# Performance work log

Measured on AMD Instinct MI355X. Metric: run time of the kernel, lower is better.

Reference implementation:

```python
import jax, jax.numpy as jnp
import numpy as np

B, S, D = 16, 4096, 64
N_HASHES, BUCKET_SIZE = 8, 64
TOKEN_SELF_ATTN_VALUE = -50000.0


def setup_inputs() -> dict:
    key = jax.random.key(0)
    k1, k2, k3 = jax.random.split(key, 3)
    qk = jax.random.normal(k1, (B, S, D), jnp.float32)
    v = jax.random.normal(k2, (B, S, D), jnp.float32)
    # random rotations for LSH hashing: (batch, dim, n_hashes, n_buckets//2)
    rotations = jax.random.normal(k3, (B, D, N_HASHES, (S // BUCKET_SIZE) // 2), jnp.float32)
    return {"qk": qk, "v": v, "rotations": rotations}


def _look_one_back(x):
    # concat each chunk with the previous chunk (wrapping): (b, c, n, ...) -> (b, c, 2n, ...)
    return jnp.concatenate([x, jnp.roll(x, 1, axis=1)], axis=2)


def _lsh_attention(qk, v, rotations):
    b, s, d = qk.shape
    n_buckets = s // BUCKET_SIZE
    # --- hash vectors (rehash_each_round=True path) ---
    rotated = jnp.einsum('btf,bfhi->bhti', qk, rotations)          # (b, h, s, nb/2)
    rotated = jnp.concatenate([rotated, -rotated], axis=-1)        # (b, h, s, nb)
    buckets = jnp.argmax(rotated, axis=-1)                          # (b, h, s)
    offsets = (jnp.arange(N_HASHES) * n_buckets)[None, :, None]
    buckets = (buckets + offsets).reshape(b, -1)                    # (b, h*s)
    # --- stable bucket sort of tokens ---
    ticker = jnp.arange(N_HASHES * s)[None, :]
    buckets_and_t = s * buckets + ticker % s
    sticker = jnp.argsort(buckets_and_t, axis=-1)                   # sorted order
    undo_sort = jnp.argsort(sticker, axis=-1)
    st = sticker % s                                                # original token index
    sqk = jnp.take_along_axis(qk, st[..., None], axis=1)            # (b, h*s, d)
    sv = jnp.take_along_axis(v, st[..., None], axis=1)
    chunk_size = N_HASHES * n_buckets
    bq_t = st.reshape(b, chunk_size, -1)                            # (b, c, n)
    bqk = sqk.reshape(b, chunk_size, -1, d)                         # (b, c, n, d)
    bv = sv.reshape(b, chunk_size, -1, d)
    # shared-QK: keys are L2-normalized queries
    norm = jnp.linalg.norm(bqk, axis=-1, keepdims=True)
    bk = bqk / jnp.maximum(norm, 1e-12)
    bk = _look_one_back(bk)                                         # (b, c, 2n, d)
    bvl = _look_one_back(bv)
    bkv_t = _look_one_back(bq_t)                                    # (b, c, 2n)
    dots = jnp.einsum('bhie,bhje->bhij', bqk, bk) * (d ** -0.5)     # (b, c, n, 2n)
    # mask self-attention (token attends to itself only as last resort)
    self_mask = bq_t[:, :, :, None] == bkv_t[:, :, None, :]
    dots = jnp.where(self_mask, TOKEN_SELF_ATTN_VALUE, dots)
    # stable softmax per chunk; keep logsumexp for cross-round combination
    lse = jax.nn.logsumexp(dots, axis=-1, keepdims=True)            # (b, c, n, 1)
    p = jnp.exp(dots - lse)
    bo = jnp.einsum('buij,buje->buie', p, bvl)                      # (b, c, n, d)
    so = bo.reshape(b, -1, d)                                       # (b, h*s, d)
    slogits = lse.reshape(b, -1)                                    # (b, h*s)
    # undo the sort
    o = jnp.take_along_axis(so, undo_sort[..., None], axis=1)
    logits = jnp.take_along_axis(slogits, undo_sort, axis=1)
    o = o.reshape(b, N_HASHES, s, d)
    logits = logits.reshape(b, N_HASHES, s, 1)
    # combine hash rounds weighted by softmax over per-round logsumexp
    probs = jnp.exp(logits - jax.nn.logsumexp(logits, axis=1, keepdims=True))
    return jnp.sum(o * probs, axis=1)                               # (b, s, d)


def reference(qk, v, rotations):
    return _lsh_attention(qk, v, rotations)
```

## Files before the change

### kernel.cpp

```cpp
#include <hip/hip_runtime.h>
#include <math.h>

#define NB_B 16
#define NB_S 4096
#define NB_D 64
#define NB_H 8

#define KSTR 72
#define PSTR 136
#define VSTR 72

typedef _Float16 half_t;
typedef __attribute__((ext_vector_type(2))) _Float16 half2t;
typedef __attribute__((ext_vector_type(4))) _Float16 half4;
typedef __attribute__((ext_vector_type(8))) _Float16 half8;
typedef __attribute__((ext_vector_type(4))) float floatx4;

__global__ __launch_bounds__(256) void prep_kernel(const float* __restrict__ qk,
                                                   const float* __restrict__ v,
                                                   half_t* __restrict__ khat,
                                                   half_t* __restrict__ vh,
                                                   float* __restrict__ norm) {
  int g = blockIdx.x * 256 + threadIdx.x;
  float4 qv = ((const float4*)qk)[g];
  float4 vv = ((const float4*)v)[g];
  float ss = qv.x * qv.x + qv.y * qv.y + qv.z * qv.z + qv.w * qv.w;
  for (int off = 1; off < 16; off <<= 1) ss += __shfl_xor(ss, off);
  float nr = fmaxf(sqrtf(ss), 1e-12f);
  float sc = 1.0f / nr;
  half4 hk = {(half_t)(qv.x * sc), (half_t)(qv.y * sc), (half_t)(qv.z * sc),
              (half_t)(qv.w * sc)};
  half4 hv = {(half_t)vv.x, (half_t)vv.y, (half_t)vv.z, (half_t)vv.w};
  ((half4*)khat)[g] = hk;
  ((half4*)vh)[g] = hv;
  if ((threadIdx.x & 15) == 0) norm[g >> 4] = nr;
}

__global__ __launch_bounds__(256) void hash_kernel(const float* __restrict__ qk,
                                                   const float* __restrict__ rot,
                                                   int* __restrict__ bkt) {
  __shared__ float rotS[64 * 32];
  int tid = threadIdx.x;
  int blk = blockIdx.x;
  int tile = blk & 15, bh = blk >> 4;
  int h = bh & 7, b = bh >> 3;
  int t = (tile << 8) + tid;

  for (int i = tid; i < 2048; i += 256) {
    int f = i >> 5, ii = i & 31;
    rotS[i] = rot[(((size_t)b * 64 + f) * 8 + h) * 32 + ii];
  }
  __syncthreads();

  const float4* qrow = (const float4*)(qk + (((size_t)b << 12) + t) * 64);
  float qreg[64];
#pragma unroll
  for (int j = 0; j < 16; j++) *(float4*)(qreg + 4 * j) = qrow[j];

  float acc[32];
#pragma unroll
  for (int i = 0; i < 32; i++) acc[i] = 0.f;

#pragma unroll
  for (int f = 0; f < 64; f++) {
    float qf = qreg[f];
#pragma unroll
    for (int i4 = 0; i4 < 8; i4++) {
      float4 w = *(const float4*)(rotS + f * 32 + i4 * 4);
      acc[i4 * 4 + 0] = __fadd_rn(acc[i4 * 4 + 0], __fmul_rn(qf, w.x));
      acc[i4 * 4 + 1] = __fadd_rn(acc[i4 * 4 + 1], __fmul_rn(qf, w.y));
      acc[i4 * 4 + 2] = __fadd_rn(acc[i4 * 4 + 2], __fmul_rn(qf, w.z));
      acc[i4 * 4 + 3] = __fadd_rn(acc[i4 * 4 + 3], __fmul_rn(qf, w.w));
    }
  }

  float b1 = acc[0];
  int i1 = 0;
#pragma unroll
  for (int i = 1; i < 32; i++)
    if (acc[i] > b1) { b1 = acc[i]; i1 = i; }
#pragma unroll
  for (int i = 0; i < 32; i++) {
    float x = -acc[i];
    if (x > b1) { b1 = x; i1 = 32 + i; }
  }
  bkt[(((size_t)(b * 8 + h)) << 12) + t] = i1;
}

__global__ __launch_bounds__(256) void sort_kernel(const int* __restrict__ bkt,
                                                   int* __restrict__ st) {
  __shared__ int lb[4096];
  __shared__ int hist[4096];
  __shared__ int cumoff[64];
  int tid = threadIdx.x;
  int b = blockIdx.x >> 3, h = blockIdx.x & 7;
  const int* gb = bkt + (((size_t)(b * 8 + h)) << 12);
  for (int t = tid; t < 4096; t += 256) lb[t] = gb[t];
  for (int i = tid; i < 4096; i += 256) hist[i] = 0;
  __syncthreads();
  for (int t = tid; t < 4096; t += 256) atomicAdd(&hist[((t >> 6) << 6) | lb[t]], 1);
  __syncthreads();
  if (tid < 64) {
    int run = 0;
    for (int cc = 0; cc < 64; cc++) {
      int x = hist[(cc << 6) | tid];
      hist[(cc << 6) | tid] = run;
      run += x;
    }
    int s = run;
    for (int off = 1; off < 64; off <<= 1) {
      int u = __shfl_up(s, off);
      if (tid >= off) s += u;
    }
    cumoff[tid] = s - run;
  }
  __syncthreads();
  int lane = tid & 63;
  for (int p = 0; p < 16; p++) {
    int t = (p << 8) + tid;
    int vb = lb[t];
    unsigned long long m = 0xFFFFFFFFFFFFFFFFull;
#pragma unroll
    for (int bit = 0; bit < 6; bit++) {
      unsigned long long bl = __ballot((vb >> bit) & 1);
      m &= ((vb >> bit) & 1) ? bl : ~bl;
    }
    int rank = __popcll(m & ((1ull << lane) - 1ull));
    int cpos = cumoff[vb] + hist[((t >> 6) << 6) | vb] + rank;
    st[(((size_t)(b * 8 + h)) << 12) + cpos] = t;
  }
}

__global__ __launch_bounds__(256) void chunk_kernel(const half_t* __restrict__ khat,
                                                    const half_t* __restrict__ vh,
                                                    const float* __restrict__ norm,
                                                    const int* __restrict__ st,
                                                    half_t* __restrict__ oh,
                                                    float* __restrict__ lse) {
  __shared__ __align__(16) half_t Ks[128 * KSTR];
  __shared__ __align__(16) half_t Vt[64 * VSTR];
  __shared__ int tk[128];
  __shared__ float normS[64];
  int tid = threadIdx.x;
  int g = blockIdx.x & 511;
  int b = blockIdx.x >> 9;
  int h = g >> 6, c = g & 63;
  int gp = (g + 511) & 511;
  int hp = gp >> 6, cp = gp & 63;
  if (tid < 64) {
    tk[tid] = st[(((size_t)(b * 8 + h)) << 12) + (c << 6) + tid];
  } else if (tid < 128) {
    tk[tid] = st[(((size_t)(b * 8 + hp)) << 12) + (cp << 6) + (tid - 64)];
  }
  __syncthreads();
  if (tid < 64) normS[tid] = norm[(b << 12) + tk[tid]];
  for (int idx = tid; idx < 1024; idx += 256) {
    int row = idx >> 3, fo = idx & 7;
    half8 val = *(const half8*)(khat + (((size_t)(b << 12) + tk[row]) << 6) + fo * 8);
    *(half8*)(Ks + row * KSTR + fo * 8) = val;
  }
  {
    int kp = tid & 31, ch = tid >> 5;
    half8 r0 = *(const half8*)(vh + (((size_t)(b << 12) + tk[2 * kp]) << 6) + ch * 8);
    half8 r1 = *(const half8*)(vh + (((size_t)(b << 12) + tk[2 * kp + 1]) << 6) + ch * 8);
#pragma unroll
    for (int j = 0; j < 8; j++) {
      half2t pr = {r0[j], r1[j]};
      *(half2t*)(Vt + (ch * 8 + j) * VSTR + 2 * kp) = pr;
    }
  }
  __syncthreads();

  int lane = tid & 63, w = tid >> 6;
  int m = lane & 15, quad = lane >> 4;
  half8 afr[2];
#pragma unroll
  for (int ki = 0; ki < 2; ki++)
    afr[ki] = *(const half8*)(Ks + (w * 16 + m) * KSTR + ki * 32 + quad * 8);
  int ti[4];
  float scr[4];
#pragma unroll
  for (int r = 0; r < 4; r++) {
    int rr = w * 16 + quad * 4 + r;
    ti[r] = tk[rr];
    scr[r] = 0.125f * normS[rr];
  }

  float d[8][4];
#pragma unroll
  for (int nt = 0; nt < 8; nt++) {
    floatx4 acc = {0.f, 0.f, 0.f, 0.f};
#pragma unroll
    for (int ki = 0; ki < 2; ki++) {
      half8 bfr = *(const half8*)(Ks + (nt * 16 + m) * KSTR + ki * 32 + quad * 8);
      acc = __builtin_amdgcn_mfma_f32_16x16x32_f16(afr[ki], bfr, acc, 0, 0, 0);
    }
    int tj = tk[nt * 16 + m];
#pragma unroll
    for (int r = 0; r < 4; r++)
      d[nt][r] = (ti[r] == tj) ? -50000.0f : acc[r] * scr[r];
  }

  float mr[4], lr[4];
#pragma unroll
  for (int r = 0; r < 4; r++) {
    float mm = d[0][r];
#pragma unroll
    for (int nt = 1; nt < 8; nt++) mm = fmaxf(mm, d[nt][r]);
    for (int off = 1; off < 16; off <<= 1) mm = fmaxf(mm, __shfl_xor(mm, off));
    float ll = 0.f;
#pragma unroll
    for (int nt = 0; nt < 8; nt++) ll += __expf(d[nt][r] - mm);
    for (int off = 1; off < 16; off <<= 1) ll += __shfl_xor(ll, off);
    mr[r] = mm;
    lr[r] = ll;
    if (m == 0) lse[(((size_t)(b * 8 + h)) << 12) + ti[r]] = mm + __logf(ll);
  }
  __syncthreads();

  half_t* Ps = Ks;
#pragma unroll
  for (int nt = 0; nt < 8; nt++) {
#pragma unroll
    for (int r = 0; r < 4; r++) {
      Ps[(w * 16 + quad * 4 + r) * PSTR + nt * 16 + m] = (half_t)__expf(d[nt][r] - mr[r]);
    }
  }
  __syncthreads();

  half8 pfr[4];
#pragma unroll
  for (int kk = 0; kk < 4; kk++)
    pfr[kk] = *(const half8*)(Ps + (w * 16 + m) * PSTR + kk * 32 + quad * 8);

  floatx4 accO[4];
#pragma unroll
  for (int dt = 0; dt < 4; dt++) accO[dt] = (floatx4){0.f, 0.f, 0.f, 0.f};

#pragma unroll
  for (int dt = 0; dt < 4; dt++) {
#pragma unroll
    for (int kk = 0; kk < 2; kk++) {
      half8 bfr = *(const half8*)(Vt + (dt * 16 + m) * VSTR + kk * 32 + quad * 8);
      accO[dt] = __builtin_amdgcn_mfma_f32_16x16x32_f16(pfr[kk], bfr, accO[dt], 0, 0, 0);
    }
  }
  __syncthreads();

  {
    int kp = tid & 31, ch = tid >> 5;
    half8 r0 = *(const half8*)(vh + (((size_t)(b << 12) + tk[64 + 2 * kp]) << 6) + ch * 8);
    half8 r1 = *(const half8*)(vh + (((size_t)(b << 12) + tk[65 + 2 * kp]) << 6) + ch * 8);
#pragma unroll
    for (int j = 0; j < 8; j++) {
      half2t pr = {r0[j], r1[j]};
      *(half2t*)(Vt + (ch * 8 + j) * VSTR + 2 * kp) = pr;
    }
  }
  __syncthreads();

#pragma unroll
  for (int dt = 0; dt < 4; dt++) {
#pragma unroll
    for (int kk = 2; kk < 4; kk++) {
      half8 bfr = *(const half8*)(Vt + (dt * 16 + m) * VSTR + (kk - 2) * 32 + quad * 8);
      accO[dt] = __builtin_amdgcn_mfma_f32_16x16x32_f16(pfr[kk], bfr, accO[dt], 0, 0, 0);
    }
  }
  __syncthreads();

  half_t* Ot = Vt;
#pragma unroll
  for (int r = 0; r < 4; r++) {
    float inv = 1.0f / lr[r];
#pragma unroll
    for (int dt = 0; dt < 4; dt++) {
      Ot[(w * 16 + quad * 4 + r) * VSTR + dt * 16 + m] = (half_t)(accO[dt][r] * inv);
    }
  }
  __syncthreads();
  for (int idx = tid; idx < 512; idx += 256) {
    int row = idx >> 3, fo = idx & 7;
    half8 val = *(const half8*)(Ot + row * VSTR + fo * 8);
    *(half8*)(oh + ((((size_t)(b * 8 + h)) << 12) + tk[row]) * 64 + fo * 8) = val;
  }
}

__global__ __launch_bounds__(256) void combine_kernel(const half_t* __restrict__ oh,
                                                      const float* __restrict__ lse,
                                                      float* __restrict__ out) {
  int idx = blockIdx.x * 256 + threadIdx.x;
  int do8 = idx & 7;
  int ts = idx >> 3;
  int b = ts >> 12, t = ts & 4095;
  size_t base = ((size_t)b << 15) + t;
  float L[8];
  float m = -3.4e38f;
#pragma unroll
  for (int h = 0; h < 8; h++) {
    L[h] = lse[base + ((size_t)h << 12)];
    m = fmaxf(m, L[h]);
  }
  float s = 0.f;
#pragma unroll
  for (int h = 0; h < 8; h++) s += __expf(L[h] - m);
  float lt = m + __logf(s);
  float acc[8];
#pragma unroll
  for (int j = 0; j < 8; j++) acc[j] = 0.f;
#pragma unroll
  for (int h = 0; h < 8; h++) {
    float wgt = __expf(L[h] - lt);
    half8 o = *(const half8*)(oh + ((base + ((size_t)h << 12)) << 6) + do8 * 8);
#pragma unroll
    for (int j = 0; j < 8; j++) acc[j] += wgt * (float)o[j];
  }
  float* dst = out + ((((size_t)b << 12) + t) << 6) + do8 * 8;
  *(float4*)dst = (float4){acc[0], acc[1], acc[2], acc[3]};
  *(float4*)(dst + 4) = (float4){acc[4], acc[5], acc[6], acc[7]};
}

extern "C" void kernel_launch(void* const* d_in, const int* in_sizes, int n_in,
                              void* d_out, int out_size, void* d_ws, size_t ws_size,
                              hipStream_t stream) {
  const float* qk = (const float*)d_in[0];
  const float* v = (const float*)d_in[1];
  const float* rot = (const float*)d_in[2];
  float* out = (float*)d_out;

  int* bkt = (int*)d_ws;
  int* stp = bkt + NB_B * NB_H * NB_S;
  float* lse = (float*)(stp + NB_B * NB_H * NB_S);
  float* norm = lse + NB_B * NB_H * NB_S;
  half_t* khat = (half_t*)(norm + NB_B * NB_S);
  half_t* vh = khat + (size_t)NB_B * NB_S * NB_D;
  half_t* oh = vh + (size_t)NB_B * NB_S * NB_D;

  prep_kernel<<<NB_B * NB_S * 16 / 256, 256, 0, stream>>>(qk, v, khat, vh, norm);
  hash_kernel<<<NB_B * NB_H * 16, 256, 0, stream>>>(qk, rot, bkt);
  sort_kernel<<<NB_B * NB_H, 256, 0, stream>>>(bkt, stp);
  chunk_kernel<<<NB_B * 512, 256, 0, stream>>>(khat, vh, norm, stp, oh, lse);
  combine_kernel<<<NB_B * NB_S * 8 / 256, 256, 0, stream>>>(oh, lse, out);
}
```

Baseline: 214.3 us.

## Preload both V halves, dedupe softmax exps, and hash two rounds per block

The chunk kernel now loads both halves of the look-back V tile into separate LDS buffers up front. This removes a mid-kernel global load and two barriers, and the redundant barrier after the per-wave P store is dropped. Softmax exponentials are computed once and reused for the row sum and the P matrix instead of being evaluated twice. The hash kernel handles two hash rounds per block, reusing the query registers and reading rotations straight from global memory with uniform addresses instead of staging them in LDS. In exchange it uses about 9 KB more LDS per chunk block and launches half as many hash blocks.

```diff
diff --git a/kernel.cpp b/kernel.cpp
--- a/kernel.cpp
+++ b/kernel.cpp
@@ -39,52 +39,52 @@
 __global__ __launch_bounds__(256) void hash_kernel(const float* __restrict__ qk,
                                                    const float* __restrict__ rot,
                                                    int* __restrict__ bkt) {
-  __shared__ float rotS[64 * 32];
   int tid = threadIdx.x;
   int blk = blockIdx.x;
-  int tile = blk & 15, bh = blk >> 4;
-  int h = bh & 7, b = bh >> 3;
+  int tile = blk & 15;
+  int bhp = blk >> 4;
+  int hp = bhp & 3, b = bhp >> 2;
   int t = (tile << 8) + tid;
-
-  for (int i = tid; i < 2048; i += 256) {
-    int f = i >> 5, ii = i & 31;
-    rotS[i] = rot[(((size_t)b * 64 + f) * 8 + h) * 32 + ii];
-  }
-  __syncthreads();
 
   const float4* qrow = (const float4*)(qk + (((size_t)b << 12) + t) * 64);
   float qreg[64];
 #pragma unroll
   for (int j = 0; j < 16; j++) *(float4*)(qreg + 4 * j) = qrow[j];
 
-  float acc[32];
-#pragma unroll
-  for (int i = 0; i < 32; i++) acc[i] = 0.f;
-
-#pragma unroll
-  for (int f = 0; f < 64; f++) {
-    float qf = qreg[f];
-#pragma unroll
-    for (int i4 = 0; i4 < 8; i4++) {
-      float4 w = *(const float4*)(rotS + f * 32 + i4 * 4);
-      acc[i4 * 4 + 0] = __fadd_rn(acc[i4 * 4 + 0], __fmul_rn(qf, w.x));
-      acc[i4 * 4 + 1] = __fadd_rn(acc[i4 * 4 + 1], __fmul_rn(qf, w.y));
-      acc[i4 * 4 + 2] = __fadd_rn(acc[i4 * 4 + 2], __fmul_rn(qf, w.z));
-      acc[i4 * 4 + 3] = __fadd_rn(acc[i4 * 4 + 3], __fmul_rn(qf, w.w));
-    }
-  }
-
-  float b1 = acc[0];
-  int i1 = 0;
-#pragma unroll
-  for (int i = 1; i < 32; i++)
-    if (acc[i] > b1) { b1 = acc[i]; i1 = i; }
-#pragma unroll
-  for (int i = 0; i < 32; i++) {
-    float x = -acc[i];
-    if (x > b1) { b1 = x; i1 = 32 + i; }
-  }
-  bkt[(((size_t)(b * 8 + h)) << 12) + t] = i1;
+#pragma unroll 1
+  for (int hh = 0; hh < 2; hh++) {
+    int h = hp * 2 + hh;
+    const float* rw = rot + (size_t)b * 16384 + h * 32;
+
+    float acc[32];
+#pragma unroll
+    for (int i = 0; i < 32; i++) acc[i] = 0.f;
+
+#pragma unroll
+    for (int f = 0; f < 64; f++) {
+      float qf = qreg[f];
+#pragma unroll
+      for (int i4 = 0; i4 < 8; i4++) {
+        float4 w = *(const float4*)(rw + f * 256 + i4 * 4);
+        acc[i4 * 4 + 0] = __fadd_rn(acc[i4 * 4 + 0], __fmul_rn(qf, w.x));
+        acc[i4 * 4 + 1] = __fadd_rn(acc[i4 * 4 + 1], __fmul_rn(qf, w.y));
+        acc[i4 * 4 + 2] = __fadd_rn(acc[i4 * 4 + 2], __fmul_rn(qf, w.z));
+        acc[i4 * 4 + 3] = __fadd_rn(acc[i4 * 4 + 3], __fmul_rn(qf, w.w));
+      }
+    }
+
+    float b1 = acc[0];
+    int i1 = 0;
+#pragma unroll
+    for (int i = 1; i < 32; i++)
+      if (acc[i] > b1) { b1 = acc[i]; i1 = i; }
+#pragma unroll
+    for (int i = 0; i < 32; i++) {
+      float x = -acc[i];
+      if (x > b1) { b1 = x; i1 = 32 + i; }
+    }
+    bkt[(((size_t)(b * 8 + h)) << 12) + t] = i1;
+  }
 }
 
 __global__ __launch_bounds__(256) void sort_kernel(const int* __restrict__ bkt,
@@ -138,7 +138,8 @@
                                                     half_t* __restrict__ oh,
                                                     float* __restrict__ lse) {
   __shared__ __align__(16) half_t Ks[128 * KSTR];
-  __shared__ __align__(16) half_t Vt[64 * VSTR];
+  __shared__ __align__(16) half_t Vt0[64 * VSTR];
+  __shared__ __align__(16) half_t Vt1[64 * VSTR];
   __shared__ int tk[128];
   __shared__ float normS[64];
   int tid = threadIdx.x;
@@ -163,10 +164,14 @@
     int kp = tid & 31, ch = tid >> 5;
     half8 r0 = *(const half8*)(vh + (((size_t)(b << 12) + tk[2 * kp]) << 6) + ch * 8);
     half8 r1 = *(const half8*)(vh + (((size_t)(b << 12) + tk[2 * kp + 1]) << 6) + ch * 8);
+    half8 r2 = *(const half8*)(vh + (((size_t)(b << 12) + tk[64 + 2 * kp]) << 6) + ch * 8);
+    half8 r3 = *(const half8*)(vh + (((size_t)(b << 12) + tk[65 + 2 * kp]) << 6) + ch * 8);
 #pragma unroll
     for (int j = 0; j < 8; j++) {
-      half2t pr = {r0[j], r1[j]};
-      *(half2t*)(Vt + (ch * 8 + j) * VSTR + 2 * kp) = pr;
+      half2t p0 = {r0[j], r1[j]};
+      half2t p1 = {r2[j], r3[j]};
+      *(half2t*)(Vt0 + (ch * 8 + j) * VSTR + 2 * kp) = p0;
+      *(half2t*)(Vt1 + (ch * 8 + j) * VSTR + 2 * kp) = p1;
     }
   }
   __syncthreads();
@@ -201,20 +206,27 @@
       d[nt][r] = (ti[r] == tj) ? -50000.0f : acc[r] * scr[r];
   }
 
-  float mr[4], lr[4];
+  float mr4[4], lr4[4];
 #pragma unroll
   for (int r = 0; r < 4; r++) {
     float mm = d[0][r];
 #pragma unroll
     for (int nt = 1; nt < 8; nt++) mm = fmaxf(mm, d[nt][r]);
     for (int off = 1; off < 16; off <<= 1) mm = fmaxf(mm, __shfl_xor(mm, off));
+    mr4[r] = mm;
+  }
+#pragma unroll
+  for (int nt = 0; nt < 8; nt++)
+#pragma unroll
+    for (int r = 0; r < 4; r++) d[nt][r] = __expf(d[nt][r] - mr4[r]);
+#pragma unroll
+  for (int r = 0; r < 4; r++) {
     float ll = 0.f;
 #pragma unroll
-    for (int nt = 0; nt < 8; nt++) ll += __expf(d[nt][r] - mm);
+    for (int nt = 0; nt < 8; nt++) ll += d[nt][r];
     for (int off = 1; off < 16; off <<= 1) ll += __shfl_xor(ll, off);
-    mr[r] = mm;
-    lr[r] = ll;
-    if (m == 0) lse[(((size_t)(b * 8 + h)) << 12) + ti[r]] = mm + __logf(ll);
+    lr4[r] = ll;
+    if (m == 0) lse[(((size_t)(b * 8 + h)) << 12) + ti[r]] = mr4[r] + __logf(ll);
   }
   __syncthreads();
 
@@ -223,10 +235,9 @@
   for (int nt = 0; nt < 8; nt++) {
 #pragma unroll
     for (int r = 0; r < 4; r++) {
-      Ps[(w * 16 + quad * 4 + r) * PSTR + nt * 16 + m] = (half_t)__expf(d[nt][r] - mr[r]);
-    }
-  }
-  __syncthreads();
+      Ps[(w * 16 + quad * 4 + r) * PSTR + nt * 16 + m] = (half_t)d[nt][r];
+    }
+  }
 
   half8 pfr[4];
 #pragma unroll
@@ -241,38 +252,21 @@
   for (int dt = 0; dt < 4; dt++) {
 #pragma unroll
     for (int kk = 0; kk < 2; kk++) {
-      half8 bfr = *(const half8*)(Vt + (dt * 16 + m) * VSTR + kk * 32 + quad * 8);
+      half8 bfr = *(const half8*)(Vt0 + (dt * 16 + m) * VSTR + kk * 32 + quad * 8);
       accO[dt] = __builtin_amdgcn_mfma_f32_16x16x32_f16(pfr[kk], bfr, accO[dt], 0, 0, 0);
     }
-  }
-  __syncthreads();
-
-  {
-    int kp = tid & 31, ch = tid >> 5;
-    half8 r0 = *(const half8*)(vh + (((size_t)(b << 12) + tk[64 + 2 * kp]) << 6) + ch * 8);
-    half8 r1 = *(const half8*)(vh + (((size_t)(b << 12) + tk[65 + 2 * kp]) << 6) + ch * 8);
-#pragma unroll
-    for (int j = 0; j < 8; j++) {
-      half2t pr = {r0[j], r1[j]};
-      *(half2t*)(Vt + (ch * 8 + j) * VSTR + 2 * kp) = pr;
-    }
-  }
-  __syncthreads();
-
-#pragma unroll
-  for (int dt = 0; dt < 4; dt++) {
 #pragma unroll
     for (int kk = 2; kk < 4; kk++) {
-      half8 bfr = *(const half8*)(Vt + (dt * 16 + m) * VSTR + (kk - 2) * 32 + quad * 8);
+      half8 bfr = *(const half8*)(Vt1 + (dt * 16 + m) * VSTR + (kk - 2) * 32 + quad * 8);
       accO[dt] = __builtin_amdgcn_mfma_f32_16x16x32_f16(pfr[kk], bfr, accO[dt], 0, 0, 0);
     }
   }
   __syncthreads();
 
-  half_t* Ot = Vt;
+  half_t* Ot = Vt0;
 #pragma unroll
   for (int r = 0; r < 4; r++) {
-    float inv = 1.0f / lr[r];
+    float inv = 1.0f / lr4[r];
 #pragma unroll
     for (int dt = 0; dt < 4; dt++) {
       Ot[(w * 16 + quad * 4 + r) * VSTR + dt * 16 + m] = (half_t)(accO[dt][r] * inv);
@@ -337,7 +331,7 @@
   half_t* oh = vh + (size_t)NB_B * NB_S * NB_D;
 
   prep_kernel<<<NB_B * NB_S * 16 / 256, 256, 0, stream>>>(qk, v, khat, vh, norm);
-  hash_kernel<<<NB_B * NB_H * 16, 256, 0, stream>>>(qk, rot, bkt);
+  hash_kernel<<<NB_B * 4 * 16, 256, 0, stream>>>(qk, rot, bkt);
   sort_kernel<<<NB_B * NB_H, 256, 0, stream>>>(bkt, stp);
   chunk_kernel<<<NB_B * 512, 256, 0, stream>>>(khat, vh, norm, stp, oh, lse);
   combine_kernel<<<NB_B * NB_S * 8 / 256, 256, 0, stream>>>(oh, lse, out);
```

Result: slower. 584.0 us (+172.5%).
